# Kernel tuning notes

Hardware: AMD Instinct MI355X
Metric: run time of the kernel (lower is better)

Reference implementation:

```python
import jax, jax.numpy as jnp
import numpy as np

B, T, E = 16, 1024, 1024
G, N, D = 4, 8, 128
V = 2048


def setup_inputs() -> dict:
    key = jax.random.key(0)
    k1, k2, k3, k4 = jax.random.split(key, 4)
    x_emb = jax.random.normal(k1, (B, T, E), dtype=jnp.float32)
    W_in = jax.random.normal(k2, (E, G * N * D), dtype=jnp.float32) / np.sqrt(E)
    R = jax.random.normal(k3, (G, N, D, D), dtype=jnp.float32) / np.sqrt(D)
    b = jnp.zeros((G, N, D), dtype=jnp.float32)
    W_proj = jax.random.normal(k4, (V, N * D), dtype=jnp.float32) / np.sqrt(D)
    b_proj = jnp.zeros((V,), dtype=jnp.float32)
    return {"x_emb": x_emb, "W_in": W_in, "R": R, "b": b, "W_proj": W_proj, "b_proj": b_proj}


def reference(x_emb, W_in, R, b, W_proj, b_proj):
    # Input projection for all timesteps at once: [B,T,G,N,D]
    Bx, Tx, Ex = x_emb.shape
    Wx = jnp.einsum('bte,eg->btg', x_emb, W_in).reshape(Bx, Tx, G, N, D)

    def step(carry, wx_t):
        h, c = carry  # [B,N,D] each
        # per-head matrix recurrence: R[g] @ h  -> [B,G,N,D]
        gates = wx_t + jnp.einsum('gnde,bne->bgnd', R, h) + b
        i = jax.nn.sigmoid(gates[:, 0])
        f = jax.nn.sigmoid(gates[:, 1])
        z = jnp.tanh(gates[:, 2])
        o = jax.nn.sigmoid(gates[:, 3])
        c_new = f * c + i * z
        h_new = o * jnp.tanh(c_new)
        return (h_new, c_new), h_new

    h0 = jnp.zeros((Bx, N, D), dtype=x_emb.dtype)
    c0 = jnp.zeros((Bx, N, D), dtype=x_emb.dtype)
    (hN, cN), hs = jax.lax.scan(step, (h0, c0), jnp.swapaxes(Wx, 0, 1))  # hs: [T,B,N,D]
    h_flat = jnp.swapaxes(hs, 0, 1).reshape(Bx, Tx, N * D)
    logits = jnp.einsum('btn,vn->btv', h_flat, W_proj) + b_proj
    return logits
```

## Files before the change

### kernel.cpp

```cpp
#include <hip/hip_runtime.h>
#include <hip/hip_bf16.h>

#define DEV __device__ __forceinline__

using bf16 = __hip_bfloat16;
typedef __attribute__((ext_vector_type(8))) short short8v;
typedef __attribute__((ext_vector_type(4))) float f32x4;

constexpr int Bq = 16, Tq = 1024, Eq = 1024, Gq = 4, Nq = 8, Dq = 128, Vq = 2048;
constexpr int M1 = Bq * Tq;
constexpr int N1q = Gq * Nq * Dq;
constexpr int K1 = Eq;
constexpr int K2 = Nq * Dq;
constexpr int N2 = Vq;

DEV unsigned short bfu(float x) {
  union { bf16 h; unsigned short u; } cv;
  cv.h = __float2bfloat16(x);
  return cv.u;
}

DEV float rcp_(float x) { return __builtin_amdgcn_rcpf(x); }
DEV float sigm(float x) { return rcp_(1.0f + __expf(-x)); }
DEV float tanh_(float x) { return fmaf(2.0f, rcp_(1.0f + __expf(-2.0f * x)), -1.0f); }

#define GLD16(gp, lp)                                                       \
  __builtin_amdgcn_global_load_lds(                                        \
      (const __attribute__((address_space(1))) void*)(gp),                 \
      (__attribute__((address_space(3))) void*)(lp), 16, 0, 0)

#define SBAR0() __builtin_amdgcn_sched_barrier(0)
#define RAWBAR()                                                            \
  do { SBAR0(); __builtin_amdgcn_s_barrier(); SBAR0(); } while (0)
#define VMW6() asm volatile("s_waitcnt vmcnt(6)" ::: "memory")
#define VMW3() asm volatile("s_waitcnt vmcnt(3)" ::: "memory")
#define VMW0() asm volatile("s_waitcnt vmcnt(0)" ::: "memory")

__global__ __launch_bounds__(256) void cast_f32_bf16(const float* __restrict__ s,
                                                     bf16* __restrict__ d, int n4) {
  const int i = blockIdx.x * 256 + threadIdx.x;
  if (i >= n4) return;
  const float4 v = ((const float4*)s)[i];
  ushort4 u;
  u.x = bfu(v.x); u.y = bfu(v.y); u.z = bfu(v.z); u.w = bfu(v.w);
  ((ushort4*)d)[i] = u;
}

__global__ __launch_bounds__(256) void transpose_cast_perm(const float* __restrict__ s,
                                                           bf16* __restrict__ d,
                                                           int SK, int SN) {
  __shared__ float t[32][33];
  const int n0 = blockIdx.x * 32, k0 = blockIdx.y * 32;
  const int tx = threadIdx.x & 31, ty = threadIdx.x >> 5;
#pragma unroll
  for (int i = 0; i < 32; i += 8)
    t[ty + i][tx] = s[(size_t)(k0 + ty + i) * SN + n0 + tx];
  __syncthreads();
#pragma unroll
  for (int i = 0; i < 32; i += 8) {
    const int c = n0 + ty + i;
    const int g = c >> 10, n = (c >> 7) & 7, dd = c & 127;
    const int rp = n * 512 + dd * 4 + g;
    d[(size_t)rp * SK + k0 + tx] = __float2bfloat16(t[tx][ty + i]);
  }
}

__global__ __launch_bounds__(256) void zero_flags(unsigned int* __restrict__ f) {
  f[blockIdx.x * 256 + threadIdx.x] = 0u;
}

__global__ __launch_bounds__(256) void gemm_out(const bf16* __restrict__ A,
                                                const bf16* __restrict__ Bt,
                                                float* __restrict__ C,
                                                const float* __restrict__ bp,
                                                int K, int N) {
  __shared__ bf16 As[128 * 32];
  __shared__ bf16 Bs[128 * 32];
  const int m0 = blockIdx.y * 128, n0 = blockIdx.x * 128;
  const int tid = threadIdx.x;
  const int lane = tid & 63, w = tid >> 6;
  const int wm = w >> 1, wn = w & 1;

  const int srow = lane >> 2, scol = (lane & 3) * 8;
  const int ca = w * 2;
  const bf16* Ag0 = A + (size_t)(m0 + ca * 16 + srow) * K + scol;
  const bf16* Ag1 = Ag0 + (size_t)16 * K;
  const bf16* Bg0 = Bt + (size_t)(n0 + ca * 16 + srow) * K + scol;
  const bf16* Bg1 = Bg0 + (size_t)16 * K;
  bf16* Al0 = As + ca * 512;
  bf16* Al1 = Al0 + 512;
  bf16* Bl0 = Bs + ca * 512;
  bf16* Bl1 = Bl0 + 512;

  f32x4 acc[4][4] = {};
  const int rr = lane & 15;
  const int kb = (lane >> 4) * 8;

  for (int k0 = 0; k0 < K; k0 += 32) {
    GLD16(Ag0 + k0, Al0);
    GLD16(Ag1 + k0, Al1);
    GLD16(Bg0 + k0, Bl0);
    GLD16(Bg1 + k0, Bl1);
    __syncthreads();
    short8v af[4], bfr[4];
#pragma unroll
    for (int i = 0; i < 4; ++i) {
      af[i]  = *(const short8v*)&As[(wm * 64 + i * 16 + rr) * 32 + kb];
      bfr[i] = *(const short8v*)&Bs[(wn * 64 + i * 16 + rr) * 32 + kb];
    }
#pragma unroll
    for (int i = 0; i < 4; ++i)
#pragma unroll
      for (int j = 0; j < 4; ++j)
        acc[i][j] = __builtin_amdgcn_mfma_f32_16x16x32_bf16(af[i], bfr[j], acc[i][j], 0, 0, 0);
    __syncthreads();
  }

  const int crow = (lane >> 4) * 4, ccol = lane & 15;
  float bv[4];
#pragma unroll
  for (int j = 0; j < 4; ++j) bv[j] = bp[n0 + wn * 64 + j * 16 + ccol];
#pragma unroll
  for (int i = 0; i < 4; ++i)
#pragma unroll
    for (int j = 0; j < 4; ++j) {
      const size_t base =
          (size_t)(m0 + wm * 64 + i * 16 + crow) * N + (n0 + wn * 64 + j * 16 + ccol);
#pragma unroll
      for (int jj = 0; jj < 4; ++jj)
        C[base + (size_t)jj * N] = acc[i][j][jj] + bv[j];
    }
}

__global__ __launch_bounds__(512) void fused_xw_lstm(
    const bf16* __restrict__ xb, const bf16* __restrict__ WiT,
    bf16* __restrict__ Wx, const float* __restrict__ bp,
    const float* __restrict__ R, bf16* __restrict__ h_all,
    unsigned int* flags) {
  __shared__ bf16 Ab[4][128 * 32];
  __shared__ bf16 Bb[4][2][128 * 32];
  __shared__ __align__(16) unsigned short hl[2][4][144];

  const int bid = blockIdx.x;
  const int tid = threadIdx.x;

  auto produce_pair = [&](int pi) {
    const int lane = tid & 63;
    const int w8 = tid >> 6;
    const int ts = w8 >> 2;
    const int w4 = w8 & 3;
    const int wm = w4 >> 1, wn = w4 & 1;
    const int rr = lane & 15, kb = (lane >> 4) * 8;
    const int crow = (lane >> 4) * 4, ccol = lane & 15;
    const int frow = 16 * w8 + (lane >> 2);
    const int fcol = (lane & 3) * 8;
    bf16* const Adst = &Ab[0][16 * w8 * 32];
    bf16* const B0dst = &Bb[0][0][16 * w8 * 32];
    bf16* const B1dst = &Bb[0][1][16 * w8 * 32];

    const int tix0 = pi * 2;
    const int s = tix0 >> 9;
    const int rem = tix0 & 511;
    const int bn = rem >> 2, q0 = rem & 3;
    const int b = bn >> 3, n = bn & 7;
    const int m0 = (b * 8 + s) * 128;
    const int n0base = (n * 4 + q0) * 128;

    const bf16* Asrc = xb + (size_t)(m0 + frow) * 1024 + fcol;
    const bf16* B0src = WiT + (size_t)(n0base + frow) * 1024 + fcol;
    const bf16* B1src = B0src + (size_t)128 * 1024;

#define FILLCHUNK(BUF, KC)                                                   \
  do {                                                                       \
    const size_t go_ = (size_t)(KC) * 32;                                    \
    GLD16(Asrc + go_, Adst + (BUF) * 4096);                                  \
    GLD16(B0src + go_, B0dst + (BUF) * 8192);                                \
    GLD16(B1src + go_, B1dst + (BUF) * 8192);                                \
  } while (0)

    f32x4 acc[4][4] = {};

#define COMPUTECHUNK(BUF)                                                    \
  do {                                                                       \
    const bf16* Ap_ = &Ab[(BUF)][0];                                         \
    const bf16* Bp_ = &Bb[(BUF)][ts][0];                                     \
    short8v af[4], bfr[4];                                                   \
    _Pragma("unroll") for (int i2 = 0; i2 < 4; ++i2) {                       \
      af[i2]  = *(const short8v*)&Ap_[(wm * 64 + i2 * 16 + rr) * 32 + kb];   \
      bfr[i2] = *(const short8v*)&Bp_[(wn * 64 + i2 * 16 + rr) * 32 + kb];   \
    }                                                                        \
    _Pragma("unroll") for (int i2 = 0; i2 < 4; ++i2)                         \
      _Pragma("unroll") for (int j2 = 0; j2 < 4; ++j2)                       \
        acc[i2][j2] = __builtin_amdgcn_mfma_f32_16x16x32_bf16(               \
            af[i2], bfr[j2], acc[i2][j2], 0, 0, 0);                          \
  } while (0)

    FILLCHUNK(0, 0);
    FILLCHUNK(1, 1);
    for (int i = 0; i < 30; ++i) {
      FILLCHUNK((i + 2) & 3, i + 2);
      VMW6();
      RAWBAR();
      COMPUTECHUNK(i & 3);
    }
    VMW3();
    RAWBAR();
    COMPUTECHUNK(2);
    VMW0();
    RAWBAR();
    COMPUTECHUNK(3);

    {
      const int n0t = n0base + ts * 128;
#pragma unroll
      for (int i = 0; i < 4; ++i)
#pragma unroll
        for (int j = 0; j < 4; ++j) {
          const int pc = n0t + wn * 64 + j * 16 + ccol;
          const int nn = pc >> 9, gd = pc & 511;
          const int g = gd & 3, dd = gd >> 2;
          const float bvj = bp[(g * 8 + nn) * 128 + dd];
#pragma unroll
          for (int jj = 0; jj < 4; ++jj) {
            const int row = m0 + wm * 64 + i * 16 + crow + jj;
            const int bb = row >> 10, t = row & 1023;
            const size_t idx = (((size_t)(bb * 8 + nn) << 10) + t) * 512 + gd;
            Wx[idx] = __float2bfloat16(acc[i][j][jj] + bvj);
          }
        }
    }
    __syncthreads();
    if (tid == 0) {
      __threadfence();
      __hip_atomic_fetch_add(&flags[bn * 8 + s], 2u,
                             __ATOMIC_RELEASE, __HIP_MEMORY_SCOPE_AGENT);
    }
#undef FILLCHUNK
#undef COMPUTECHUNK
  };

  produce_pair(bid);

  if (bid < 224) {
    for (int pi = 256 + bid; pi < 2048; pi += 224) produce_pair(pi);
  } else {
    const int cid = bid - 224;
    const int n = cid & 7, bq = cid >> 3;
    const int w = tid >> 6, lane = tid & 63;
    const int lg = lane >> 4, lc = lane & 15;
    const int bloc = lc & 3;
    const int ci = lc >> 2;
    const int dsite = 16 * w + 4 * ci + lg;

    short8v Af[4][4];
#pragma unroll
    for (int tau = 0; tau < 4; ++tau) {
      const int gd = 64 * w + 16 * tau + lc;
      const int g = gd & 3, d = gd >> 2;
      const float* rbase = R + ((size_t)(g * 8 + n) * 128 + d) * 128;
#pragma unroll
      for (int kf = 0; kf < 4; ++kf) {
        const float* rp = rbase + 32 * kf + 8 * lg;
        const float4 r0 = *(const float4*)rp;
        const float4 r1 = *(const float4*)(rp + 4);
        short8v bv;
        bv[0] = (short)bfu(r0.x); bv[1] = (short)bfu(r0.y);
        bv[2] = (short)bfu(r0.z); bv[3] = (short)bfu(r0.w);
        bv[4] = (short)bfu(r1.x); bv[5] = (short)bfu(r1.y);
        bv[6] = (short)bfu(r1.z); bv[7] = (short)bfu(r1.w);
        Af[tau][kf] = bv;
      }
    }

    for (int i = tid; i < 4 * 144; i += 512) (&hl[0][0][0])[i] = 0;
    __syncthreads();

    const bf16* wxb =
        Wx + ((size_t)((bq * 4 + bloc) * 8 + n) << 10) * 512 + dsite * 4;
    bf16* hout = h_all + ((size_t)(bq * 4 + bloc) << 20) + n * 128 + dsite;

    float c = 0.f;

    for (int s = 0; s < 8; ++s) {
      if (tid == 0) {
#pragma unroll
        for (int j = 0; j < 4; ++j) {
          const int fidx = ((bq * 4 + j) * 8 + n) * 8 + s;
          while (__hip_atomic_load(&flags[fidx], __ATOMIC_RELAXED,
                                   __HIP_MEMORY_SCOPE_AGENT) < 4u)
            __builtin_amdgcn_s_sleep(2);
        }
        __threadfence();
      }
      __syncthreads();

      ushort4 wxr[4];
#pragma unroll
      for (int u = 0; u < 4; ++u)
        wxr[u] = *(const ushort4*)(wxb + (size_t)(s * 128 + u) * 512);

      const int tend = s * 128 + 128;
      for (int t0 = s * 128; t0 < tend; t0 += 4) {
#pragma unroll
        for (int u = 0; u < 4; ++u) {
          const int t = t0 + u;
          const unsigned short* hb = &hl[t & 1][0][0];
          short8v Bf[4];
#pragma unroll
          for (int kf = 0; kf < 4; ++kf)
            Bf[kf] = *(const short8v*)(hb + bloc * 144 + kf * 32 + lg * 8);

          const ushort4 wxc = wxr[u];

          f32x4 acc[4];
#pragma unroll
          for (int tau = 0; tau < 4; ++tau) {
            acc[tau][0] = 0.f; acc[tau][1] = 0.f;
            acc[tau][2] = 0.f; acc[tau][3] = 0.f;
          }
#pragma unroll
          for (int kf = 0; kf < 4; ++kf)
#pragma unroll
            for (int tau = 0; tau < 4; ++tau)
              acc[tau] = __builtin_amdgcn_mfma_f32_16x16x32_bf16(
                  Af[tau][kf], Bf[kf], acc[tau], 0, 0, 0);

          {
            const int tp = (t + 4 < tend) ? (t + 4) : (tend - 1);
            wxr[u] = *(const ushort4*)(wxb + (size_t)tp * 512);
          }

          float pre0 = (ci & 2) ? ((ci & 1) ? acc[3][0] : acc[2][0])
                                : ((ci & 1) ? acc[1][0] : acc[0][0]);
          float pre1 = (ci & 2) ? ((ci & 1) ? acc[3][1] : acc[2][1])
                                : ((ci & 1) ? acc[1][1] : acc[0][1]);
          float pre2 = (ci & 2) ? ((ci & 1) ? acc[3][2] : acc[2][2])
                                : ((ci & 1) ? acc[1][2] : acc[0][2]);
          float pre3 = (ci & 2) ? ((ci & 1) ? acc[3][3] : acc[2][3])
                                : ((ci & 1) ? acc[1][3] : acc[0][3]);
          pre0 += __uint_as_float((unsigned)wxc.x << 16);
          pre1 += __uint_as_float((unsigned)wxc.y << 16);
          pre2 += __uint_as_float((unsigned)wxc.z << 16);
          pre3 += __uint_as_float((unsigned)wxc.w << 16);

          const float i_ = sigm(pre0);
          const float f_ = sigm(pre1);
          const float z_ = tanh_(pre2);
          const float o_ = sigm(pre3);
          c = f_ * c + i_ * z_;
          const float h = o_ * tanh_(c);
          const bf16 h16 = __float2bfloat16(h);

          hl[(t + 1) & 1][bloc][dsite] = ((const unsigned short*)&h16)[0];
          hout[(size_t)t << 10] = h16;

          __builtin_amdgcn_sched_barrier(0);
          asm volatile("s_waitcnt lgkmcnt(0)" ::: "memory");
          __builtin_amdgcn_sched_barrier(0);
          __builtin_amdgcn_s_barrier();
          __builtin_amdgcn_sched_barrier(0);
        }
      }
    }
  }
}

extern "C" void kernel_launch(void* const* d_in, const int* in_sizes, int n_in,
                              void* d_out, int out_size, void* d_ws, size_t ws_size,
                              hipStream_t stream) {
  const float* x_emb = (const float*)d_in[0];
  const float* W_in  = (const float*)d_in[1];
  const float* R     = (const float*)d_in[2];
  const float* bias  = (const float*)d_in[3];
  const float* W_prj = (const float*)d_in[4];
  const float* b_prj = (const float*)d_in[5];

  char* ws = (char*)d_ws;
  bf16* xb  = (bf16*)ws;
  bf16* WiT = (bf16*)(ws + (size_t)M1 * K1 * 2);
  bf16* Wpb = WiT + (size_t)N1q * K1;
  bf16* H   = Wpb + (size_t)N2 * K2;
  unsigned int* flags = (unsigned int*)(ws + ((size_t)76 << 20));
  bf16* Wx = (bf16*)d_out;

  cast_f32_bf16<<<(M1 * K1 / 4 + 255) / 256, 256, 0, stream>>>(x_emb, xb, M1 * K1 / 4);
  transpose_cast_perm<<<dim3(N1q / 32, K1 / 32), 256, 0, stream>>>(W_in, WiT, K1, N1q);
  cast_f32_bf16<<<(N2 * K2 / 4 + 255) / 256, 256, 0, stream>>>(W_prj, Wpb, N2 * K2 / 4);
  zero_flags<<<4, 256, 0, stream>>>(flags);

  fused_xw_lstm<<<dim3(256), dim3(512), 0, stream>>>(xb, WiT, Wx, bias, R, H, flags);

  gemm_out<<<dim3(N2 / 128, M1 / 128), 256, 0, stream>>>(
      H, Wpb, (float*)d_out, b_prj, K2, N2);
}
```

Measured before the change: 755.0 us.

## Fuse output projection into LSTM kernel, overlapping it with the recurrence via flags

Producer blocks that finish computing the input projection now also compute output-projection tiles for each 128-step chunk once the recurrent blocks signal, through new per-chunk h flags, that those hidden states are written. This overlaps the final GEMM with the sequential recurrence instead of running it as a separate kernel afterwards. Wx moves into workspace so the output buffer can be written concurrently, and the fused path is enabled only if the workspace is large enough. Otherwise the separate gemm_out launch is kept. It adds spin-waiting and cross-block synchronization, and the projection work now competes with the producers for CUs.

```diff
diff --git a/kernel.cpp b/kernel.cpp
--- a/kernel.cpp
+++ b/kernel.cpp
@@ -136,7 +136,9 @@
     const bf16* __restrict__ xb, const bf16* __restrict__ WiT,
     bf16* __restrict__ Wx, const float* __restrict__ bp,
     const float* __restrict__ R, bf16* __restrict__ h_all,
-    unsigned int* flags) {
+    const bf16* __restrict__ Wpb, const float* __restrict__ bprj,
+    float* __restrict__ out, unsigned int* wxflags, unsigned int* hflags,
+    int do_p2) {
   __shared__ bf16 Ab[4][128 * 32];
   __shared__ bf16 Bb[4][2][128 * 32];
   __shared__ __align__(16) unsigned short hl[2][4][144];
@@ -232,7 +234,7 @@
     __syncthreads();
     if (tid == 0) {
       __threadfence();
-      __hip_atomic_fetch_add(&flags[bn * 8 + s], 2u,
+      __hip_atomic_fetch_add(&wxflags[bn * 8 + s], 2u,
                              __ATOMIC_RELEASE, __HIP_MEMORY_SCOPE_AGENT);
     }
 #undef FILLCHUNK
@@ -243,6 +245,98 @@
 
   if (bid < 224) {
     for (int pi = 256 + bid; pi < 2048; pi += 224) produce_pair(pi);
+
+    if (do_p2) {
+      const int lane = tid & 63;
+      const int w8 = tid >> 6;
+      const int ts = w8 >> 2;
+      const int w4 = w8 & 3;
+      const int wm = w4 >> 1, wn = w4 & 1;
+      const int rr = lane & 15, kb = (lane >> 4) * 8;
+      const int crow = (lane >> 4) * 4, ccol = lane & 15;
+      const int frow = 16 * w8 + (lane >> 2);
+      const int fcol = (lane & 3) * 8;
+      bf16* const Adst = &Ab[0][16 * w8 * 32];
+      bf16* const B0dst = &Bb[0][0][16 * w8 * 32];
+      bf16* const B1dst = &Bb[0][1][16 * w8 * 32];
+
+      for (int oi = bid; oi < 1024; oi += 224) {
+        const int s = oi >> 7;
+        const int rem = oi & 127;
+        const int b = rem >> 3, p = rem & 7;
+        const int m0 = b * 1024 + s * 128;
+        const int n0base = p * 256;
+
+        if (tid == 0) {
+          while (__hip_atomic_load(&hflags[b * 8 + s], __ATOMIC_RELAXED,
+                                   __HIP_MEMORY_SCOPE_AGENT) < 8u)
+            __builtin_amdgcn_s_sleep(8);
+          __threadfence();
+        }
+        __syncthreads();
+
+        const bf16* Asrc = h_all + (size_t)(m0 + frow) * 1024 + fcol;
+        const bf16* B0src = Wpb + (size_t)(n0base + frow) * 1024 + fcol;
+        const bf16* B1src = B0src + (size_t)128 * 1024;
+
+#define FILLCHUNK(BUF, KC)                                                   \
+  do {                                                                       \
+    const size_t go_ = (size_t)(KC) * 32;                                    \
+    GLD16(Asrc + go_, Adst + (BUF) * 4096);                                  \
+    GLD16(B0src + go_, B0dst + (BUF) * 8192);                                \
+    GLD16(B1src + go_, B1dst + (BUF) * 8192);                                \
+  } while (0)
+
+        f32x4 acc[4][4] = {};
+
+#define COMPUTECHUNK(BUF)                                                    \
+  do {                                                                       \
+    const bf16* Ap_ = &Ab[(BUF)][0];                                         \
+    const bf16* Bp_ = &Bb[(BUF)][ts][0];                                     \
+    short8v af[4], bfr[4];                                                   \
+    _Pragma("unroll") for (int i2 = 0; i2 < 4; ++i2) {                       \
+      af[i2]  = *(const short8v*)&Ap_[(wm * 64 + i2 * 16 + rr) * 32 + kb];   \
+      bfr[i2] = *(const short8v*)&Bp_[(wn * 64 + i2 * 16 + rr) * 32 + kb];   \
+    }                                                                        \
+    _Pragma("unroll") for (int i2 = 0; i2 < 4; ++i2)                         \
+      _Pragma("unroll") for (int j2 = 0; j2 < 4; ++j2)                       \
+        acc[i2][j2] = __builtin_amdgcn_mfma_f32_16x16x32_bf16(               \
+            af[i2], bfr[j2], acc[i2][j2], 0, 0, 0);                          \
+  } while (0)
+
+        FILLCHUNK(0, 0);
+        FILLCHUNK(1, 1);
+        for (int i = 0; i < 30; ++i) {
+          FILLCHUNK((i + 2) & 3, i + 2);
+          VMW6();
+          RAWBAR();
+          COMPUTECHUNK(i & 3);
+        }
+        VMW3();
+        RAWBAR();
+        COMPUTECHUNK(2);
+        VMW0();
+        RAWBAR();
+        COMPUTECHUNK(3);
+
+        {
+          const int n0t = n0base + ts * 128;
+#pragma unroll
+          for (int i = 0; i < 4; ++i)
+#pragma unroll
+            for (int j = 0; j < 4; ++j) {
+              const int col = n0t + wn * 64 + j * 16 + ccol;
+              const float bvj = bprj[col];
+#pragma unroll
+              for (int jj = 0; jj < 4; ++jj)
+                out[(size_t)(m0 + wm * 64 + i * 16 + crow + jj) * N2 + col] =
+                    acc[i][j][jj] + bvj;
+            }
+        }
+#undef FILLCHUNK
+#undef COMPUTECHUNK
+      }
+    }
   } else {
     const int cid = bid - 224;
     const int n = cid & 7, bq = cid >> 3;
@@ -286,7 +380,7 @@
 #pragma unroll
         for (int j = 0; j < 4; ++j) {
           const int fidx = ((bq * 4 + j) * 8 + n) * 8 + s;
-          while (__hip_atomic_load(&flags[fidx], __ATOMIC_RELAXED,
+          while (__hip_atomic_load(&wxflags[fidx], __ATOMIC_RELAXED,
                                    __HIP_MEMORY_SCOPE_AGENT) < 4u)
             __builtin_amdgcn_s_sleep(2);
         }
@@ -361,6 +455,15 @@
           __builtin_amdgcn_sched_barrier(0);
         }
       }
+
+      __syncthreads();
+      if (tid == 0) {
+        __threadfence();
+#pragma unroll
+        for (int j = 0; j < 4; ++j)
+          __hip_atomic_fetch_add(&hflags[(bq * 4 + j) * 8 + s], 1u,
+                                 __ATOMIC_RELEASE, __HIP_MEMORY_SCOPE_AGENT);
+      }
     }
   }
 }
@@ -381,15 +484,25 @@
   bf16* Wpb = WiT + (size_t)N1q * K1;
   bf16* H   = Wpb + (size_t)N2 * K2;
   unsigned int* flags = (unsigned int*)(ws + ((size_t)76 << 20));
-  bf16* Wx = (bf16*)d_out;
+  unsigned int* wxflags = flags;
+  unsigned int* hflags  = flags + 1024;
+
+  const size_t wxBytes = (size_t)M1 * N1q * 2;
+  const size_t wxOff = (size_t)80 << 20;
+  const bool big = ws_size >= wxOff + wxBytes;
+  bf16* Wx = big ? (bf16*)(ws + wxOff) : (bf16*)d_out;
+  const int do_p2 = big ? 1 : 0;
 
   cast_f32_bf16<<<(M1 * K1 / 4 + 255) / 256, 256, 0, stream>>>(x_emb, xb, M1 * K1 / 4);
   transpose_cast_perm<<<dim3(N1q / 32, K1 / 32), 256, 0, stream>>>(W_in, WiT, K1, N1q);
   cast_f32_bf16<<<(N2 * K2 / 4 + 255) / 256, 256, 0, stream>>>(W_prj, Wpb, N2 * K2 / 4);
-  zero_flags<<<4, 256, 0, stream>>>(flags);
-
-  fused_xw_lstm<<<dim3(256), dim3(512), 0, stream>>>(xb, WiT, Wx, bias, R, H, flags);
-
-  gemm_out<<<dim3(N2 / 128, M1 / 128), 256, 0, stream>>>(
-      H, Wpb, (float*)d_out, b_prj, K2, N2);
-}
+  zero_flags<<<5, 256, 0, stream>>>(flags);
+
+  fused_xw_lstm<<<dim3(256), dim3(512), 0, stream>>>(
+      xb, WiT, Wx, bias, R, H, Wpb, b_prj, (float*)d_out, wxflags, hflags, do_p2);
+
+  if (!do_p2) {
+    gemm_out<<<dim3(N2 / 128, M1 / 128), 256, 0, stream>>>(
+        H, Wpb, (float*)d_out, b_prj, K2, N2);
+  }
+}
```

After: 799.9 us. 6.0% more time.
